# Kernel tuning notes

Measured on AMD Instinct MI355X. Metric: run time of the kernel, lower is better.

The kernel has to match this reference:

```python
import jax, jax.numpy as jnp
import numpy as np

THR = 1.0
ALPHA = 5.0
C = 0.4
TAU_U = 20.0
DT = 1.0

def slayer(x):
    # SE-adlif SLAYER surrogate: c*alpha / (2*exp(alpha*|x|))
    return C * ALPHA / (2.0 * jnp.exp(jnp.abs(x) * ALPHA))

def setup_inputs() -> dict:
    key = jax.random.key(0)
    k1, k2, k3 = jax.random.split(key, 3)
    B, T, IN, OUT = 64, 1000, 512, 512
    x = jax.random.normal(k1, (B, T, IN), dtype=jnp.float32)
    lim = 1.0 / np.sqrt(IN)
    weight = jax.random.uniform(k2, (OUT, IN), minval=-lim, maxval=lim, dtype=jnp.float32)
    bias = jnp.zeros((OUT,), jnp.float32)
    # orthogonal init for recurrent weights
    recurrent = jnp.linalg.qr(jax.random.normal(k3, (OUT, OUT), dtype=jnp.float32))[0].astype(jnp.float32)
    # fixed tau trainer: decay = exp(-dt/tau)
    decay = jnp.full((OUT,), np.exp(-DT / TAU_U), dtype=jnp.float32)
    return {"input_tensor": x, "weight": weight, "bias": bias, "recurrent": recurrent, "decay": decay}

def reference(input_tensor, weight, bias, recurrent, decay):
    B = input_tensor.shape[0]
    OUT = weight.shape[0]
    sg = jax.lax.stop_gradient
    # precompute input-driven current for all timesteps: [B, T, OUT]
    cur = jnp.einsum('bti,oi->bto', input_tensor, weight) + bias
    v0 = jnp.zeros((B, OUT), jnp.float32)
    z0 = jnp.zeros((B, OUT), jnp.float32)

    def step(carry, c_t):
        v_tm1, z_tm1 = carry
        v_tm1 = v_tm1 * (1.0 - sg(z_tm1))  # detached reset
        soma = c_t + z_tm1 @ recurrent.T
        v_t = decay * v_tm1 + (1.0 - decay) * soma
        v_thr = v_t - THR
        hv = jnp.where(v_thr >= 0, 1.0, 0.0).astype(v_thr.dtype)
        # straight-through: value = heaviside, grad = SLAYER surrogate
        z_t = sg(hv) + (v_thr - sg(v_thr)) * sg(slayer(v_thr))
        return (v_t, z_t), (v_t, z_t)

    _, (vs, zs) = jax.lax.scan(step, (v0, z0), jnp.swapaxes(cur, 0, 1))
    vs = jnp.swapaxes(vs, 0, 1)  # [B, T, OUT]
    zs = jnp.swapaxes(zs, 0, 1)
    v_full = jnp.concatenate([v0[:, None], vs], axis=1)  # [B, T+1, OUT]
    z_full = jnp.concatenate([z0[:, None], zs], axis=1)
    states = jnp.stack([v_full, z_full], axis=0)  # [2, B, T+1, OUT]
    outputs = zs  # [B, T, OUT]
    return outputs, states
```

## Files before the change

### kernel.cpp

```cpp
#include <hip/hip_runtime.h>

#define SV_OFF 32768000
#define SZ_OFF 65568768

typedef __attribute__((ext_vector_type(8))) short bf16x8;
typedef __attribute__((ext_vector_type(4))) float f32x4;

__device__ __forceinline__ unsigned short f2bf(float f) {
  union { float f; unsigned u; } x; x.f = f;
  unsigned r = x.u + 0x7fffu + ((x.u >> 16) & 1u);
  return (unsigned short)(r >> 16);
}

__device__ __forceinline__ void gl_lds16(const void* g, void* l) {
  __builtin_amdgcn_global_load_lds(
      (const __attribute__((address_space(1))) unsigned int*)g,
      (__attribute__((address_space(3))) unsigned int*)l, 16, 0, 0);
}

__global__ __launch_bounds__(256) void prep(const float* __restrict__ W,
                                            unsigned short* __restrict__ Wb,
                                            int* __restrict__ flags) {
  const int idx = blockIdx.x * 256 + threadIdx.x;
  if (idx < 512 * 512) Wb[idx] = f2bf(W[idx]);
  if (idx < 64) flags[idx] = 0;
}

__global__ __launch_bounds__(256) void cvt_x(const float* __restrict__ x,
                                             unsigned short* __restrict__ xb) {
  const size_t i = ((size_t)blockIdx.x * 256 + threadIdx.x) * 8;
  const float4 a = *(const float4*)(x + i);
  const float4 b = *(const float4*)(x + i + 4);
  bf16x8 h;
  h[0] = (short)f2bf(a.x); h[1] = (short)f2bf(a.y);
  h[2] = (short)f2bf(a.z); h[3] = (short)f2bf(a.w);
  h[4] = (short)f2bf(b.x); h[5] = (short)f2bf(b.y);
  h[6] = (short)f2bf(b.z); h[7] = (short)f2bf(b.w);
  *(bf16x8*)(xb + i) = h;
}

__global__ __launch_bounds__(640, 1) void fused(
    const unsigned short* __restrict__ Ab,
    const unsigned short* __restrict__ Wb,
    const float* __restrict__ bias,
    const float* __restrict__ decay,
    float* __restrict__ out,
    int* __restrict__ flags) {
  __shared__ unsigned short As[4][128][32];
  __shared__ unsigned short Bs[4][128][32];
  __shared__ float cs[128][128];

  const int b    = blockIdx.x;
  const int o0   = blockIdx.y * 128;
  const int tid  = threadIdx.x;
  const int lane = tid & 63;
  const int wave = tid >> 6;
  const bool gemm = tid < 512;
  const int lr = lane & 15;
  const int lq = lane >> 4;
  const int wr = (wave >> 2) & 1;
  const int wc = wave & 3;

  const int row0 = tid >> 2;
  const int scol = ((tid & 3) * 16) ^ ((row0 & 3) << 4);
  const char* abase = (const char*)Ab + (size_t)b * 1000 * 1024;
  const char* bbase = (const char*)Wb + (size_t)o0 * 1024;

#define STAGE(s_) do {                                                          \
    const int t0_ = ((s_) >> 4) * 128;                                          \
    const int kb_ = ((s_) & 15) * 64;                                           \
    const int bf_ = (s_) & 3;                                                   \
    gl_lds16(abase + (size_t)(t0_ + row0) * 1024 + kb_ + scol,                  \
             (char*)&As[bf_][0][0] + tid * 16);                                 \
    gl_lds16(bbase + (size_t)row0 * 1024 + kb_ + scol,                          \
             (char*)&Bs[bf_][0][0] + tid * 16);                                 \
  } while (0)

  const int so = tid - 512;
  float v = 0.f, d = 0.f, om = 0.f, bv = 0.f;
  int fl = 0;
  if (!gemm) {
    d  = decay[o0 + so];
    om = 1.f - d;
    bv = bias[o0 + so];
    __builtin_nontemporal_store(0.f, out + SV_OFF + (size_t)b * 512512 + o0 + so);
    __builtin_nontemporal_store(0.f, out + SZ_OFF + (size_t)b * 512512 + o0 + so);
  } else {
    STAGE(0); STAGE(1); STAGE(2);
  }

  int s = 0;
  for (int tile = 0; tile < 8; ++tile) {
    f32x4 acc[4][2] = {};
    for (int kk = 0; kk < 16; ++kk, ++s) {
      if (gemm)
        asm volatile("s_waitcnt vmcnt(4)" ::: "memory");
      __builtin_amdgcn_s_barrier();
      __builtin_amdgcn_sched_barrier(0);
      if (gemm) {
        STAGE((s + 3) & 127);
        const int bf_ = s & 3;
        const int fo = (lq ^ (lr & 3)) * 8;
        bf16x8 af[4], bq[2];
#pragma unroll
        for (int i = 0; i < 4; ++i)
          af[i] = *(const bf16x8*)(&As[bf_][wr * 64 + i * 16 + lr][fo]);
#pragma unroll
        for (int j = 0; j < 2; ++j)
          bq[j] = *(const bf16x8*)(&Bs[bf_][wc * 32 + j * 16 + lr][fo]);
        __builtin_amdgcn_s_setprio(1);
#pragma unroll
        for (int i = 0; i < 4; ++i)
#pragma unroll
          for (int j = 0; j < 2; ++j)
            acc[i][j] = __builtin_amdgcn_mfma_f32_16x16x32_bf16(af[i], bq[j], acc[i][j], 0, 0, 0);
        __builtin_amdgcn_s_setprio(0);
      } else if (tile > 0) {
        const int pt0 = (tile - 1) * 128;
        const int tb = kk * 8;
        float* zp = out + ((size_t)b * 1000 + pt0 + tb) * 512 + o0 + so;
        float* vp = out + SV_OFF + ((size_t)b * 1001 + pt0 + tb + 1) * 512 + o0 + so;
        float* sp = out + SZ_OFF + ((size_t)b * 1001 + pt0 + tb + 1) * 512 + o0 + so;
#pragma unroll
        for (int u = 0; u < 8; ++u) {
          const int t = tb + u;
          const float c = cs[t][so ^ (((t >> 2) & 3) << 4)];
          v = d * v + om * (c + bv);
          const float z = (v >= 1.0f) ? 1.0f : 0.0f;
          fl |= (v >= 1.0f);
          __builtin_nontemporal_store(z, zp + (size_t)u * 512);
          __builtin_nontemporal_store(v, vp + (size_t)u * 512);
          __builtin_nontemporal_store(z, sp + (size_t)u * 512);
        }
      }
    }
    __builtin_amdgcn_s_barrier();
    __builtin_amdgcn_sched_barrier(0);
    if (gemm) {
#pragma unroll
      for (int i = 0; i < 4; ++i)
#pragma unroll
        for (int j = 0; j < 2; ++j) {
          const int tb = wr * 64 + i * 16 + lq * 4;
          const int cc = (wc * 32 + j * 16 + lr) ^ (lq << 4);
#pragma unroll
          for (int r = 0; r < 4; ++r) cs[tb + r][cc] = acc[i][j][r];
        }
      asm volatile("s_waitcnt lgkmcnt(0)" ::: "memory");
    }
    __builtin_amdgcn_s_barrier();
    __builtin_amdgcn_sched_barrier(0);
  }
  if (!gemm) {
    const int pt0 = 896;
    float* zp = out + ((size_t)b * 1000 + pt0) * 512 + o0 + so;
    float* vp = out + SV_OFF + ((size_t)b * 1001 + pt0 + 1) * 512 + o0 + so;
    float* sp = out + SZ_OFF + ((size_t)b * 1001 + pt0 + 1) * 512 + o0 + so;
    for (int t = 0; t < 104; ++t) {
      const float c = cs[t][so ^ (((t >> 2) & 3) << 4)];
      v = d * v + om * (c + bv);
      const float z = (v >= 1.0f) ? 1.0f : 0.0f;
      fl |= (v >= 1.0f);
      __builtin_nontemporal_store(z, zp + (size_t)t * 512);
      __builtin_nontemporal_store(v, vp + (size_t)t * 512);
      __builtin_nontemporal_store(z, sp + (size_t)t * 512);
    }
    if (fl) atomicOr(flags + b, 1);
  }
#undef STAGE
}

__global__ __launch_bounds__(512) void scan_fix(const float* __restrict__ x,
                                                const float* __restrict__ W,
                                                const float* __restrict__ bias,
                                                const float* __restrict__ R,
                                                const float* __restrict__ decay,
                                                float* __restrict__ out,
                                                const int* __restrict__ flags) {
  const int b = blockIdx.x;
  if (flags[b] == 0) return;
  const int o = threadIdx.x;
  __shared__ float xs[512];
  __shared__ int cnt;
  __shared__ int list[512];
  const float d = decay[o];
  const float om = 1.f - d;
  float v = 0.f, z = 0.f;
  const size_t zb  = (size_t)b * 512000 + o;
  const size_t svb = (size_t)b * 512512 + o;
  float* __restrict__ sv = out + SV_OFF;
  float* __restrict__ sz = out + SZ_OFF;
  sv[svb] = 0.f;
  sz[svb] = 0.f;
  if (o == 0) cnt = 0;
  __syncthreads();
  for (int t = 0; t < 1000; ++t) {
    xs[o] = x[((size_t)b * 1000 + t) * 512 + o];
    __syncthreads();
    float soma = bias[o];
    for (int i = 0; i < 512; ++i) soma += xs[i] * W[(size_t)o * 512 + i];
    const int n = cnt;
    for (int i = 0; i < n; ++i) soma += R[(size_t)o * 512 + list[i]];
    v = d * (v * (1.f - z)) + om * soma;
    z = (v >= 1.0f) ? 1.0f : 0.0f;
    out[zb + (size_t)t * 512] = z;
    sv[svb + (size_t)(t + 1) * 512] = v;
    sz[svb + (size_t)(t + 1) * 512] = z;
    __syncthreads();
    if (o == 0) cnt = 0;
    __syncthreads();
    if (z != 0.f) { const int q = atomicAdd(&cnt, 1); list[q] = o; }
    __syncthreads();
  }
}

extern "C" void kernel_launch(void* const* d_in, const int* in_sizes, int n_in,
                              void* d_out, int out_size, void* d_ws, size_t ws_size,
                              hipStream_t stream) {
  (void)in_sizes; (void)n_in; (void)out_size; (void)ws_size;
  const float* x     = (const float*)d_in[0];
  const float* W     = (const float*)d_in[1];
  const float* bias  = (const float*)d_in[2];
  const float* R     = (const float*)d_in[3];
  const float* decay = (const float*)d_in[4];
  float* out = (float*)d_out;

  char* ws = (char*)d_ws;
  unsigned short* xb = (unsigned short*)ws;
  unsigned short* Wb = (unsigned short*)(ws + 65536000);
  int* flags         = (int*)(ws + 66060288);

  prep<<<1024, 256, 0, stream>>>(W, Wb, flags);
  cvt_x<<<16000, 256, 0, stream>>>(x, xb);
  fused<<<dim3(64, 4), 640, 0, stream>>>(xb, Wb, bias, decay, out, flags);
  scan_fix<<<64, 512, 0, stream>>>(x, W, bias, R, decay, out, flags);
}
```

Baseline: 526.9 us.

## Fuse fp32-to-bf16 input conversion into GEMM loader, drop cvt_x kernel

```diff
diff --git a/kernel.cpp b/kernel.cpp
--- a/kernel.cpp
+++ b/kernel.cpp
@@ -26,27 +26,14 @@
   if (idx < 64) flags[idx] = 0;
 }
 
-__global__ __launch_bounds__(256) void cvt_x(const float* __restrict__ x,
-                                             unsigned short* __restrict__ xb) {
-  const size_t i = ((size_t)blockIdx.x * 256 + threadIdx.x) * 8;
-  const float4 a = *(const float4*)(x + i);
-  const float4 b = *(const float4*)(x + i + 4);
-  bf16x8 h;
-  h[0] = (short)f2bf(a.x); h[1] = (short)f2bf(a.y);
-  h[2] = (short)f2bf(a.z); h[3] = (short)f2bf(a.w);
-  h[4] = (short)f2bf(b.x); h[5] = (short)f2bf(b.y);
-  h[6] = (short)f2bf(b.z); h[7] = (short)f2bf(b.w);
-  *(bf16x8*)(xb + i) = h;
-}
-
 __global__ __launch_bounds__(640, 1) void fused(
-    const unsigned short* __restrict__ Ab,
+    const float* __restrict__ x,
     const unsigned short* __restrict__ Wb,
     const float* __restrict__ bias,
     const float* __restrict__ decay,
     float* __restrict__ out,
     int* __restrict__ flags) {
-  __shared__ unsigned short As[4][128][32];
+  __shared__ unsigned short As[2][128][32];
   __shared__ unsigned short Bs[4][128][32];
   __shared__ float cs[128][128];
 
@@ -62,23 +49,31 @@
   const int wc = wave & 3;
 
   const int row0 = tid >> 2;
-  const int scol = ((tid & 3) * 16) ^ ((row0 & 3) << 4);
-  const char* abase = (const char*)Ab + (size_t)b * 1000 * 1024;
-  const char* bbase = (const char*)Wb + (size_t)o0 * 1024;
-
-#define STAGE(s_) do {                                                          \
-    const int t0_ = ((s_) >> 4) * 128;                                          \
-    const int kb_ = ((s_) & 15) * 64;                                           \
-    const int bf_ = (s_) & 3;                                                   \
-    gl_lds16(abase + (size_t)(t0_ + row0) * 1024 + kb_ + scol,                  \
-             (char*)&As[bf_][0][0] + tid * 16);                                 \
-    gl_lds16(bbase + (size_t)row0 * 1024 + kb_ + scol,                          \
-             (char*)&Bs[bf_][0][0] + tid * 16);                                 \
-  } while (0)
+  const int slot = tid & 3;
+  const int scol = (slot * 16) ^ ((row0 & 3) << 4);
+  const int awz  = row0 * 64 + ((slot ^ (row0 & 3)) * 16);
+  const float* xbase = x + (size_t)b * 512000;
+  const char*  bbase = (const char*)Wb + (size_t)o0 * 1024;
+
+#define B_STAGE(s_) do { const int ss_ = (s_) & 127;                            \
+    gl_lds16(bbase + (size_t)row0 * 1024 + (ss_ & 15) * 64 + scol,              \
+             (char*)&Bs[ss_ & 3][0][0] + tid * 16); } while (0)
+#define P_ISSUE(s_, ra, rb) do { const int ss_ = (s_) & 127;                    \
+    int rg_ = (ss_ >> 4) * 128 + row0; rg_ = rg_ > 999 ? 999 : rg_;             \
+    const float* sp_ = xbase + (size_t)rg_ * 512 + (ss_ & 15) * 32 + slot * 8;  \
+    ra = *(const float4*)sp_; rb = *(const float4*)(sp_ + 4); } while (0)
+#define A_WRITE(buf_, ra, rb) do { bf16x8 h_;                                   \
+    h_[0] = (short)f2bf(ra.x); h_[1] = (short)f2bf(ra.y);                       \
+    h_[2] = (short)f2bf(ra.z); h_[3] = (short)f2bf(ra.w);                       \
+    h_[4] = (short)f2bf(rb.x); h_[5] = (short)f2bf(rb.y);                       \
+    h_[6] = (short)f2bf(rb.z); h_[7] = (short)f2bf(rb.w);                       \
+    *(bf16x8*)((char*)&As[buf_][0][0] + awz) = h_; } while (0)
 
   const int so = tid - 512;
   float v = 0.f, d = 0.f, om = 0.f, bv = 0.f;
   int fl = 0;
+  float4 e0, e1, q0, q1;
+
   if (!gemm) {
     d  = decay[o0 + so];
     om = 1.f - d;
@@ -86,56 +81,70 @@
     __builtin_nontemporal_store(0.f, out + SV_OFF + (size_t)b * 512512 + o0 + so);
     __builtin_nontemporal_store(0.f, out + SZ_OFF + (size_t)b * 512512 + o0 + so);
   } else {
-    STAGE(0); STAGE(1); STAGE(2);
-  }
+    B_STAGE(0); B_STAGE(1); B_STAGE(2);
+    P_ISSUE(0, e0, e1);
+    asm volatile("s_waitcnt vmcnt(0)" ::: "memory");
+    A_WRITE(0, e0, e1);
+    P_ISSUE(1, q0, q1);
+    asm volatile("s_waitcnt lgkmcnt(0)" ::: "memory");
+  }
+  __builtin_amdgcn_s_barrier();
+  __builtin_amdgcn_sched_barrier(0);
+
+#define STEP_BODY(s_, iA, iB, cA, cB) do {                                      \
+    if (gemm) {                                                                 \
+      const int ab_ = (s_) & 1;                                                 \
+      const int bf_ = (s_) & 3;                                                 \
+      const int fo_ = (lq ^ (lr & 3)) * 8;                      \
+      bf16x8 af_[4], bq_[2];                                                    \
+      _Pragma("unroll")                                                         \
+      for (int i_ = 0; i_ < 4; ++i_)                                            \
+        af_[i_] = *(const bf16x8*)(&As[ab_][wr * 64 + i_ * 16 + lr][fo_]);      \
+      _Pragma("unroll")                                                         \
+      for (int j_ = 0; j_ < 2; ++j_)                                            \
+        bq_[j_] = *(const bf16x8*)(&Bs[bf_][wc * 32 + j_ * 16 + lr][fo_]);      \
+      B_STAGE((s_) + 3);                                                        \
+      P_ISSUE((s_) + 2, iA, iB);                                                \
+      __builtin_amdgcn_s_setprio(1);                                            \
+      _Pragma("unroll")                                                         \
+      for (int i_ = 0; i_ < 4; ++i_)                                            \
+        _Pragma("unroll")                                                       \
+        for (int j_ = 0; j_ < 2; ++j_)                                          \
+          acc[i_][j_] = __builtin_amdgcn_mfma_f32_16x16x32_bf16(                \
+              af_[i_], bq_[j_], acc[i_][j_], 0, 0, 0);                          \
+      __builtin_amdgcn_s_setprio(0);                                            \
+      asm volatile("s_waitcnt vmcnt(3)" ::: "memory");      \
+      A_WRITE(((s_) + 1) & 1, cA, cB);                                          \
+      asm volatile("s_waitcnt lgkmcnt(0)" ::: "memory");                        \
+    } else if (tile > 0) {                                                      \
+      const int pt0_ = (tile - 1) * 128;                                        \
+      const int tb_ = ((s_) & 15) * 8;                                          \
+      float* zp_ = out + ((size_t)b * 1000 + pt0_ + tb_) * 512 + o0 + so;       \
+      float* vp_ = out + SV_OFF + ((size_t)b * 1001 + pt0_ + tb_ + 1) * 512 + o0 + so; \
+      float* sp2_ = out + SZ_OFF + ((size_t)b * 1001 + pt0_ + tb_ + 1) * 512 + o0 + so; \
+      _Pragma("unroll")                                                         \
+      for (int u_ = 0; u_ < 8; ++u_) {                                          \
+        const int t_ = tb_ + u_;                                                \
+        const float c_ = cs[t_][so ^ (((t_ >> 2) & 3) << 4)];                   \
+        v = d * v + om * (c_ + bv);               \
+        const float z_ = (v >= 1.0f) ? 1.0f : 0.0f;                             \
+        fl |= (v >= 1.0f);                                                      \
+        __builtin_nontemporal_store(z_, zp_ + (size_t)u_ * 512);                \
+        __builtin_nontemporal_store(v,  vp_ + (size_t)u_ * 512);                \
+        __builtin_nontemporal_store(z_, sp2_ + (size_t)u_ * 512);               \
+      }                                                                         \
+    }                                                                           \
+    __builtin_amdgcn_s_barrier();                                               \
+    __builtin_amdgcn_sched_barrier(0);                                          \
+  } while (0)
 
   int s = 0;
   for (int tile = 0; tile < 8; ++tile) {
     f32x4 acc[4][2] = {};
-    for (int kk = 0; kk < 16; ++kk, ++s) {
-      if (gemm)
-        asm volatile("s_waitcnt vmcnt(4)" ::: "memory");
-      __builtin_amdgcn_s_barrier();
-      __builtin_amdgcn_sched_barrier(0);
-      if (gemm) {
-        STAGE((s + 3) & 127);
-        const int bf_ = s & 3;
-        const int fo = (lq ^ (lr & 3)) * 8;
-        bf16x8 af[4], bq[2];
-#pragma unroll
-        for (int i = 0; i < 4; ++i)
-          af[i] = *(const bf16x8*)(&As[bf_][wr * 64 + i * 16 + lr][fo]);
-#pragma unroll
-        for (int j = 0; j < 2; ++j)
-          bq[j] = *(const bf16x8*)(&Bs[bf_][wc * 32 + j * 16 + lr][fo]);
-        __builtin_amdgcn_s_setprio(1);
-#pragma unroll
-        for (int i = 0; i < 4; ++i)
-#pragma unroll
-          for (int j = 0; j < 2; ++j)
-            acc[i][j] = __builtin_amdgcn_mfma_f32_16x16x32_bf16(af[i], bq[j], acc[i][j], 0, 0, 0);
-        __builtin_amdgcn_s_setprio(0);
-      } else if (tile > 0) {
-        const int pt0 = (tile - 1) * 128;
-        const int tb = kk * 8;
-        float* zp = out + ((size_t)b * 1000 + pt0 + tb) * 512 + o0 + so;
-        float* vp = out + SV_OFF + ((size_t)b * 1001 + pt0 + tb + 1) * 512 + o0 + so;
-        float* sp = out + SZ_OFF + ((size_t)b * 1001 + pt0 + tb + 1) * 512 + o0 + so;
-#pragma unroll
-        for (int u = 0; u < 8; ++u) {
-          const int t = tb + u;
-          const float c = cs[t][so ^ (((t >> 2) & 3) << 4)];
-          v = d * v + om * (c + bv);
-          const float z = (v >= 1.0f) ? 1.0f : 0.0f;
-          fl |= (v >= 1.0f);
-          __builtin_nontemporal_store(z, zp + (size_t)u * 512);
-          __builtin_nontemporal_store(v, vp + (size_t)u * 512);
-          __builtin_nontemporal_store(z, sp + (size_t)u * 512);
-        }
-      }
+    for (int kk = 0; kk < 16; kk += 2, s += 2) {
+      STEP_BODY(s,     e0, e1, q0, q1);
+      STEP_BODY(s + 1, q0, q1, e0, e1);
     }
-    __builtin_amdgcn_s_barrier();
-    __builtin_amdgcn_sched_barrier(0);
     if (gemm) {
 #pragma unroll
       for (int i = 0; i < 4; ++i)
@@ -167,7 +176,10 @@
     }
     if (fl) atomicOr(flags + b, 1);
   }
-#undef STAGE
+#undef STEP_BODY
+#undef B_STAGE
+#undef P_ISSUE
+#undef A_WRITE
 }
 
 __global__ __launch_bounds__(512) void scan_fix(const float* __restrict__ x,
@@ -226,12 +238,10 @@
   float* out = (float*)d_out;
 
   char* ws = (char*)d_ws;
-  unsigned short* xb = (unsigned short*)ws;
-  unsigned short* Wb = (unsigned short*)(ws + 65536000);
-  int* flags         = (int*)(ws + 66060288);
+  unsigned short* Wb = (unsigned short*)ws;
+  int* flags         = (int*)(ws + 524288);
 
   prep<<<1024, 256, 0, stream>>>(W, Wb, flags);
-  cvt_x<<<16000, 256, 0, stream>>>(x, xb);
-  fused<<<dim3(64, 4), 640, 0, stream>>>(xb, Wb, bias, decay, out, flags);
+  fused<<<dim3(64, 4), 640, 0, stream>>>(x, Wb, bias, decay, out, flags);
   scan_fix<<<64, 512, 0, stream>>>(x, W, bias, R, decay, out, flags);
 }
```

New measurement: 572.9 us. 1.09x slower.
